# Kernel tuning notes

Measured on AMD Instinct MI355X. Metric: run time of the kernel, lower is better.

The kernel has to match this reference:

```python
import jax, jax.numpy as jnp
import numpy as np

B, N, D = 8, 2048, 256
TOP_K_INST = 512
TOP_K_REL = 32
EPS = 1e-5  # F.layer_norm default eps


def setup_inputs() -> dict:
    key = jax.random.key(0)
    kq, kk = jax.random.split(key)
    q = jax.random.normal(kq, (B, N, D), dtype=jnp.float32)
    k = jax.random.normal(kk, (B, N, D), dtype=jnp.float32)
    return {"q": q, "k": k}


def _forward(q, k):
    # raw attention scores [B,N,N] (returned un-normalized, like scores1 in torch)
    scores1 = jnp.einsum('bid,bjd->bij', q, k)
    probs = jax.nn.softmax(scores1, axis=-1)
    # top-k instances by softmax self-score on the diagonal, sorted ascending
    diag = jnp.diagonal(probs, axis1=-2, axis2=-1)                      # [B,N]
    inst_idx = jnp.sort(jax.lax.top_k(diag, TOP_K_INST)[1], axis=-1)    # [B,K]
    # gather selected rows then selected columns -> [B,K,K]
    sel = jnp.take_along_axis(probs, inst_idx[:, :, None], axis=1)      # [B,K,N]
    rel = jnp.take_along_axis(sel, inst_idx[:, None, :], axis=2)        # [B,K,K]
    # mask diagonal with large value (torch uses 1e9) before relationship topk
    rel = jnp.where(jnp.eye(TOP_K_INST, dtype=bool)[None, :, :], 1e9, rel)
    # top-R relationship columns per row; torch.where recovers them in
    # ascending column order, so sort to match
    rel_idx = jnp.sort(jax.lax.top_k(rel, TOP_K_REL)[1], axis=-1)       # [B,K,R]
    b, K, R = rel_idx.shape
    rows = jnp.broadcast_to(jnp.arange(K)[None, :, None], (b, K, R)).reshape(b, K * R)
    cols = rel_idx.reshape(b, K * R)
    subj = jnp.take_along_axis(inst_idx, rows, axis=-1)                 # [B,K*R]
    obj = jnp.take_along_axis(inst_idx, cols, axis=-1)                  # [B,K*R]
    batch_ids = jnp.broadcast_to(jnp.arange(b)[:, None], (b, K * R))
    soi = jnp.stack([batch_ids, subj, obj], axis=-1)                    # [B,K*R,3]
    # relationship embeds: q[subject] + q[object], then layernorm (no affine)
    subj_e = jnp.take_along_axis(q, subj[:, :, None], axis=1)           # [B,K*R,D]
    obj_e = jnp.take_along_axis(q, obj[:, :, None], axis=1)
    rel_e = subj_e + obj_e
    mu = jnp.mean(rel_e, axis=-1, keepdims=True)
    var = jnp.var(rel_e, axis=-1, keepdims=True)  # biased, matches F.layer_norm
    rel_e = (rel_e - mu) * jax.lax.rsqrt(var + EPS)
    return scores1, soi, rel_e


def reference(q, k):
    return _forward(q, k)
```

## Files before the change

### kernel.cpp

```cpp
#include <hip/hip_runtime.h>
#include <math.h>

#define BATCH 8
#define N 2048
#define D 256
#define K_INST 512
#define K_REL 32
#define PAIRS_PER_B (K_INST * K_REL)

__device__ __forceinline__ unsigned short f2h_u(float f) {
  _Float16 h = (_Float16)f;
  return __builtin_bit_cast(unsigned short, h);
}
__device__ __forceinline__ float h2f_u(unsigned short u) {
  return (float)__builtin_bit_cast(_Float16, u);
}

__global__ __launch_bounds__(256)
void split_f16(const float* __restrict__ q, const float* __restrict__ k,
               unsigned short* __restrict__ qh, unsigned short* __restrict__ ql,
               unsigned short* __restrict__ kh, unsigned short* __restrict__ kl) {
  const int E4 = BATCH * N * D / 4;
  for (int i = blockIdx.x * blockDim.x + threadIdx.x; i < 2 * E4;
       i += gridDim.x * blockDim.x) {
    const bool isK = i >= E4;
    const int j = isK ? (i - E4) : i;
    const float4 v = ((const float4*)(isK ? k : q))[j];
    ushort4 h, l;
    h.x = f2h_u(v.x); h.y = f2h_u(v.y); h.z = f2h_u(v.z); h.w = f2h_u(v.w);
    l.x = f2h_u(2048.0f * (v.x - h2f_u(h.x)));
    l.y = f2h_u(2048.0f * (v.y - h2f_u(h.y)));
    l.z = f2h_u(2048.0f * (v.z - h2f_u(h.z)));
    l.w = f2h_u(2048.0f * (v.w - h2f_u(h.w)));
    ((ushort4*)(isK ? kh : qh))[j] = h;
    ((ushort4*)(isK ? kl : ql))[j] = l;
  }
}

#define TM 128
#define TN 128
#define TK 32

typedef _Float16 f16x8 __attribute__((ext_vector_type(8)));
typedef float f32x4 __attribute__((ext_vector_type(4)));

__device__ __forceinline__ void load_lds16(const void* g, void* l) {
  __builtin_amdgcn_global_load_lds(
      (const __attribute__((address_space(1))) void*)g,
      (__attribute__((address_space(3))) void*)l, 16, 0, 0);
}

__global__ __launch_bounds__(256, 3)
void gemm_qkT_mfma(const unsigned short* __restrict__ qh,
                   const unsigned short* __restrict__ ql,
                   const unsigned short* __restrict__ kh,
                   const unsigned short* __restrict__ kl,
                   float* __restrict__ out) {
  const int bz = blockIdx.z;
  const int row0 = blockIdx.y * TM;
  const int col0 = blockIdx.x * TN;
  const size_t tb = (size_t)bz * N * D;

  __shared__ unsigned short Ah[TM * TK], Al[TM * TK], Bh[TM * TK], Bl[TM * TK];

  const int tid = threadIdx.x;
  const int lane = tid & 63;
  const int w = tid >> 6;
  const int wr = w >> 1, wc = w & 1;
  const int fr = lane & 15;
  const int g = lane >> 4;
  const int slot8 = ((g ^ (lane & 3)) << 3);

  int r_st[2], k_st[2];
#pragma unroll
  for (int i = 0; i < 2; i++) {
    const int b = ((w * 2 + i) << 10) + lane * 16;
    const int r = b >> 6;
    const int s = (b >> 4) & 3;
    r_st[i] = r;
    k_st[i] = (s ^ (r & 3)) * 8;
  }

  f32x4 acc[4][4];
#pragma unroll
  for (int m = 0; m < 4; m++)
#pragma unroll
    for (int n = 0; n < 4; n++) acc[m][n] = (f32x4){0.f, 0.f, 0.f, 0.f};
  const f32x4 zero4 = (f32x4){0.f, 0.f, 0.f, 0.f};
  const float inv2048 = 1.0f / 2048.0f;

  for (int kt = 0; kt < D; kt += TK) {
    __syncthreads();
#pragma unroll
    for (int i = 0; i < 2; i++) {
      const size_t aoff = tb + (size_t)(row0 + r_st[i]) * D + kt + k_st[i];
      const size_t boff = tb + (size_t)(col0 + r_st[i]) * D + kt + k_st[i];
      unsigned short* const la = &Ah[(w * 2 + i) * 512];
      unsigned short* const lA = &Al[(w * 2 + i) * 512];
      unsigned short* const lb = &Bh[(w * 2 + i) * 512];
      unsigned short* const lB = &Bl[(w * 2 + i) * 512];
      load_lds16(qh + aoff, la);
      load_lds16(ql + aoff, lA);
      load_lds16(kh + boff, lb);
      load_lds16(kl + boff, lB);
    }
    __syncthreads();

    f16x8 ah[4], al[4];
#pragma unroll
    for (int m = 0; m < 4; m++) {
      const int idx = (wr * 64 + m * 16 + fr) * TK + slot8;
      ah[m] = *(const f16x8*)&Ah[idx];
      al[m] = *(const f16x8*)&Al[idx];
    }
#pragma unroll
    for (int n = 0; n < 4; n++) {
      const int idx = (wc * 64 + n * 16 + fr) * TK + slot8;
      const f16x8 bhf = *(const f16x8*)&Bh[idx];
      const f16x8 blf = *(const f16x8*)&Bl[idx];
#pragma unroll
      for (int m = 0; m < 4; m++) {
        f32x4 t = __builtin_amdgcn_mfma_f32_16x16x32_f16(ah[m], blf, zero4, 0, 0, 0);
        t = __builtin_amdgcn_mfma_f32_16x16x32_f16(al[m], bhf, t, 0, 0, 0);
        acc[m][n] = __builtin_amdgcn_mfma_f32_16x16x32_f16(ah[m], bhf, acc[m][n], 0, 0, 0);
        acc[m][n] += t * inv2048;
      }
    }
  }

  float* O = out + (size_t)bz * N * N;
#pragma unroll
  for (int m = 0; m < 4; m++) {
#pragma unroll
    for (int r4 = 0; r4 < 4; r4++) {
      float* orow =
          &O[(size_t)(row0 + wr * 64 + m * 16 + g * 4 + r4) * N + col0 + wc * 64 + fr];
#pragma unroll
      for (int n = 0; n < 4; n++) orow[n * 16] = acc[m][n][r4];
    }
  }
}

__global__ __launch_bounds__(256)
void row_stats(const float* __restrict__ scores, float* __restrict__ m_out,
               float* __restrict__ s_out, float* __restrict__ diag_out) {
  const int row = blockIdx.x;
  const float* srow = scores + (size_t)row * N;
  const float4* r4 = (const float4*)srow;
  const int t = threadIdx.x;
  const int lane = t & 63, wid = t >> 6;
  float4 v0 = r4[t];
  float4 v1 = r4[t + 256];
  float mx = fmaxf(fmaxf(fmaxf(v0.x, v0.y), fmaxf(v0.z, v0.w)),
                   fmaxf(fmaxf(v1.x, v1.y), fmaxf(v1.z, v1.w)));
  __shared__ float redm[4], reds[4], bc[1];
#pragma unroll
  for (int o = 32; o > 0; o >>= 1) mx = fmaxf(mx, __shfl_down(mx, o));
  if (lane == 0) redm[wid] = mx;
  __syncthreads();
  if (t == 0) bc[0] = fmaxf(fmaxf(redm[0], redm[1]), fmaxf(redm[2], redm[3]));
  __syncthreads();
  const float m = bc[0];
  float s = expf(v0.x - m) + expf(v0.y - m) + expf(v0.z - m) + expf(v0.w - m)
          + expf(v1.x - m) + expf(v1.y - m) + expf(v1.z - m) + expf(v1.w - m);
#pragma unroll
  for (int o = 32; o > 0; o >>= 1) s += __shfl_down(s, o);
  if (lane == 0) reds[wid] = s;
  __syncthreads();
  if (t == 0) {
    float S = reds[0] + reds[1] + reds[2] + reds[3];
    int i = row & (N - 1);
    float sii = srow[i];
    m_out[row] = m;
    s_out[row] = S;
    diag_out[row] = expf(sii - m) / S;
  }
}

__global__ __launch_bounds__(1024)
void topk_inst(const float* __restrict__ diag, int* __restrict__ inst) {
  const int b = blockIdx.x;
  __shared__ float v[2048];
  __shared__ int id[2048];
  __shared__ int sel[K_INST];
  const int tid = threadIdx.x;
  for (int e = tid; e < 2048; e += 1024) { v[e] = diag[b * N + e]; id[e] = e; }
  __syncthreads();
  for (int k = 2; k <= 2048; k <<= 1) {
    for (int j = k >> 1; j > 0; j >>= 1) {
      const int p = tid;
      int i = 2 * p - (p & (j - 1));
      int ixj = i | j;
      float va = v[i], vb = v[ixj];
      int ia = id[i], ib = id[ixj];
      bool a_first = (va > vb) || (va == vb && ia < ib);
      bool up = ((i & k) == 0);
      if (up != a_first) { v[i] = vb; v[ixj] = va; id[i] = ib; id[ixj] = ia; }
      __syncthreads();
    }
  }
  if (tid < K_INST) sel[tid] = id[tid];
  __syncthreads();
  for (int k = 2; k <= K_INST; k <<= 1) {
    for (int j = k >> 1; j > 0; j >>= 1) {
      if (tid < 256) {
        int p = tid;
        int i = 2 * p - (p & (j - 1));
        int ixj = i | j;
        int a = sel[i], c = sel[ixj];
        bool a_first = a < c;
        bool up = ((i & k) == 0);
        if (up != a_first) { sel[i] = c; sel[ixj] = a; }
      }
      __syncthreads();
    }
  }
  if (tid < K_INST) inst[b * K_INST + tid] = sel[tid];
}

__global__ __launch_bounds__(256)
void rel_topk(const float* __restrict__ scores, const float* __restrict__ m_arr,
              const float* __restrict__ s_arr, const int* __restrict__ inst,
              float* __restrict__ soi_out, int* __restrict__ pairs) {
  const int blk = blockIdx.x;
  const int b = blk >> 9;
  const int r = blk & 511;
  __shared__ float v[K_INST];
  __shared__ int c[K_INST];
  __shared__ int selc[K_REL];
  __shared__ int sortedc[K_REL];
  const int tid = threadIdx.x;
  const int subj = inst[b * K_INST + r];
  const int rowg = b * N + subj;
  const float m = m_arr[rowg];
  const float S = s_arr[rowg];
  const float* srow = scores + (size_t)rowg * N;
  for (int e = tid; e < K_INST; e += 256) {
    int col = inst[b * K_INST + e];
    v[e] = (e == r) ? 1e9f : expf(srow[col] - m) / S;
    c[e] = e;
  }
  __syncthreads();
  for (int k = 2; k <= K_INST; k <<= 1) {
    for (int j = k >> 1; j > 0; j >>= 1) {
      int p = tid;
      int i = 2 * p - (p & (j - 1));
      int ixj = i | j;
      float va = v[i], vb = v[ixj];
      int ia = c[i], ib = c[ixj];
      bool a_first = (va > vb) || (va == vb && ia < ib);
      bool up = ((i & k) == 0);
      if (up != a_first) { v[i] = vb; v[ixj] = va; c[i] = ib; c[ixj] = ia; }
      __syncthreads();
    }
  }
  if (tid < K_REL) selc[tid] = c[tid];
  __syncthreads();
  if (tid < K_REL) {
    int myc = selc[tid];
    int rank = 0;
#pragma unroll
    for (int p2 = 0; p2 < K_REL; p2++) rank += (selc[p2] < myc);
    sortedc[rank] = myc;
  }
  __syncthreads();
  if (tid < K_REL) {
    int cc = sortedc[tid];
    int obj = inst[b * K_INST + cc];
    size_t pidx = (size_t)b * PAIRS_PER_B + (size_t)r * K_REL + tid;
    soi_out[pidx * 3 + 0] = (float)b;
    soi_out[pidx * 3 + 1] = (float)subj;
    soi_out[pidx * 3 + 2] = (float)obj;
    pairs[pidx * 2 + 0] = subj;
    pairs[pidx * 2 + 1] = obj;
  }
}

__global__ __launch_bounds__(256)
void rel_embed(const float* __restrict__ q, const int* __restrict__ pairs,
               float* __restrict__ out) {
  const size_t p = (size_t)blockIdx.x * 4 + (threadIdx.x >> 6);
  const int lane = threadIdx.x & 63;
  const int b = (int)(p >> 14);
  const int subj = pairs[p * 2], obj = pairs[p * 2 + 1];
  const float* qs = q + ((size_t)b * N + subj) * D;
  const float* qo = q + ((size_t)b * N + obj) * D;
  const float4 a = *(const float4*)(qs + lane * 4);
  const float4 c = *(const float4*)(qo + lane * 4);
  float4 e = make_float4(a.x + c.x, a.y + c.y, a.z + c.z, a.w + c.w);
  float s = e.x + e.y + e.z + e.w;
#pragma unroll
  for (int o = 32; o > 0; o >>= 1) s += __shfl_down(s, o);
  const float mu = __shfl(s, 0) * (1.0f / D);
  float4 dv = make_float4(e.x - mu, e.y - mu, e.z - mu, e.w - mu);
  float s2 = dv.x * dv.x + dv.y * dv.y + dv.z * dv.z + dv.w * dv.w;
#pragma unroll
  for (int o = 32; o > 0; o >>= 1) s2 += __shfl_down(s2, o);
  const float var = __shfl(s2, 0) * (1.0f / D);
  const float r = rsqrtf(var + 1e-5f);
  *(float4*)(out + p * D + lane * 4) =
      make_float4(dv.x * r, dv.y * r, dv.z * r, dv.w * r);
}

extern "C" void kernel_launch(void* const* d_in, const int* in_sizes, int n_in,
                              void* d_out, int out_size, void* d_ws, size_t ws_size,
                              hipStream_t stream) {
  const float* q = (const float*)d_in[0];
  const float* k = (const float*)d_in[1];
  float* out = (float*)d_out;

  float* scores = out;
  float* soi = out + (size_t)BATCH * N * N;
  float* rele = soi + (size_t)BATCH * PAIRS_PER_B * 3;

  float* m_arr = (float*)d_ws;
  float* s_arr = m_arr + BATCH * N;
  float* diag = s_arr + BATCH * N;
  int* inst = (int*)(diag + BATCH * N);
  int* pairs = inst + BATCH * K_INST;

  unsigned short* qh = (unsigned short*)rele;
  unsigned short* ql = qh + (size_t)BATCH * N * D;
  unsigned short* kh = ql + (size_t)BATCH * N * D;
  unsigned short* kl = kh + (size_t)BATCH * N * D;

  split_f16<<<4096, 256, 0, stream>>>(q, k, qh, ql, kh, kl);
  gemm_qkT_mfma<<<dim3(N / TN, N / TM, BATCH), 256, 0, stream>>>(qh, ql, kh, kl, scores);
  row_stats<<<BATCH * N, 256, 0, stream>>>(scores, m_arr, s_arr, diag);
  topk_inst<<<BATCH, 1024, 0, stream>>>(diag, inst);
  rel_topk<<<BATCH * K_INST, 256, 0, stream>>>(scores, m_arr, s_arr, inst, soi, pairs);
  rel_embed<<<BATCH * PAIRS_PER_B / 4, 256, 0, stream>>>(q, pairs, rele);
}
```

Measured before the change: 423.5 us.

## Fold split-f16 scaling into a pre-scaled Q copy and sort raw-score keys

The split-precision GEMM now stores an extra Q high-part copy pre-scaled by 2048. All three MFMAs can then accumulate into a single accumulator, with one rescale at the store, instead of a temporary chain plus a vector multiply-add per tile. This costs extra global traffic and LDS for the fifth operand. The relationship top-k now sorts packed 64-bit order-preserving keys built from raw scores, since softmax is monotonic per row, which drops the exp/divide and the separate index arrays.

```diff
diff --git a/kernel.cpp b/kernel.cpp
--- a/kernel.cpp
+++ b/kernel.cpp
@@ -18,8 +18,9 @@
 
 __global__ __launch_bounds__(256)
 void split_f16(const float* __restrict__ q, const float* __restrict__ k,
-               unsigned short* __restrict__ qh, unsigned short* __restrict__ ql,
-               unsigned short* __restrict__ kh, unsigned short* __restrict__ kl) {
+               unsigned short* __restrict__ qhs, unsigned short* __restrict__ qh,
+               unsigned short* __restrict__ ql, unsigned short* __restrict__ kh,
+               unsigned short* __restrict__ kl) {
   const int E4 = BATCH * N * D / 4;
   for (int i = blockIdx.x * blockDim.x + threadIdx.x; i < 2 * E4;
        i += gridDim.x * blockDim.x) {
@@ -32,8 +33,19 @@
     l.y = f2h_u(2048.0f * (v.y - h2f_u(h.y)));
     l.z = f2h_u(2048.0f * (v.z - h2f_u(h.z)));
     l.w = f2h_u(2048.0f * (v.w - h2f_u(h.w)));
-    ((ushort4*)(isK ? kh : qh))[j] = h;
-    ((ushort4*)(isK ? kl : ql))[j] = l;
+    if (isK) {
+      ((ushort4*)kh)[j] = h;
+      ((ushort4*)kl)[j] = l;
+    } else {
+      ushort4 hs;
+      hs.x = f2h_u(2048.0f * h2f_u(h.x));
+      hs.y = f2h_u(2048.0f * h2f_u(h.y));
+      hs.z = f2h_u(2048.0f * h2f_u(h.z));
+      hs.w = f2h_u(2048.0f * h2f_u(h.w));
+      ((ushort4*)qhs)[j] = hs;
+      ((ushort4*)qh)[j] = h;
+      ((ushort4*)ql)[j] = l;
+    }
   }
 }
 
@@ -51,7 +63,8 @@
 }
 
 __global__ __launch_bounds__(256, 3)
-void gemm_qkT_mfma(const unsigned short* __restrict__ qh,
+void gemm_qkT_mfma(const unsigned short* __restrict__ qhs,
+                   const unsigned short* __restrict__ qh,
                    const unsigned short* __restrict__ ql,
                    const unsigned short* __restrict__ kh,
                    const unsigned short* __restrict__ kl,
@@ -61,7 +74,8 @@
   const int col0 = blockIdx.x * TN;
   const size_t tb = (size_t)bz * N * D;
 
-  __shared__ unsigned short Ah[TM * TK], Al[TM * TK], Bh[TM * TK], Bl[TM * TK];
+  __shared__ unsigned short Ahs[TM * TK], Ah[TM * TK], Al[TM * TK],
+                            Bh[TM * TK], Bl[TM * TK];
 
   const int tid = threadIdx.x;
   const int lane = tid & 63;
@@ -86,8 +100,6 @@
   for (int m = 0; m < 4; m++)
 #pragma unroll
     for (int n = 0; n < 4; n++) acc[m][n] = (f32x4){0.f, 0.f, 0.f, 0.f};
-  const f32x4 zero4 = (f32x4){0.f, 0.f, 0.f, 0.f};
-  const float inv2048 = 1.0f / 2048.0f;
 
   for (int kt = 0; kt < D; kt += TK) {
     __syncthreads();
@@ -95,21 +107,20 @@
     for (int i = 0; i < 2; i++) {
       const size_t aoff = tb + (size_t)(row0 + r_st[i]) * D + kt + k_st[i];
       const size_t boff = tb + (size_t)(col0 + r_st[i]) * D + kt + k_st[i];
-      unsigned short* const la = &Ah[(w * 2 + i) * 512];
-      unsigned short* const lA = &Al[(w * 2 + i) * 512];
-      unsigned short* const lb = &Bh[(w * 2 + i) * 512];
-      unsigned short* const lB = &Bl[(w * 2 + i) * 512];
-      load_lds16(qh + aoff, la);
-      load_lds16(ql + aoff, lA);
-      load_lds16(kh + boff, lb);
-      load_lds16(kl + boff, lB);
+      const int ldsoff = (w * 2 + i) * 512;
+      load_lds16(qhs + aoff, &Ahs[ldsoff]);
+      load_lds16(qh  + aoff, &Ah[ldsoff]);
+      load_lds16(ql  + aoff, &Al[ldsoff]);
+      load_lds16(kh  + boff, &Bh[ldsoff]);
+      load_lds16(kl  + boff, &Bl[ldsoff]);
     }
     __syncthreads();
 
-    f16x8 ah[4], al[4];
+    f16x8 ahs[4], ah[4], al[4];
 #pragma unroll
     for (int m = 0; m < 4; m++) {
       const int idx = (wr * 64 + m * 16 + fr) * TK + slot8;
+      ahs[m] = *(const f16x8*)&Ahs[idx];
       ah[m] = *(const f16x8*)&Ah[idx];
       al[m] = *(const f16x8*)&Al[idx];
     }
@@ -120,15 +131,15 @@
       const f16x8 blf = *(const f16x8*)&Bl[idx];
 #pragma unroll
       for (int m = 0; m < 4; m++) {
-        f32x4 t = __builtin_amdgcn_mfma_f32_16x16x32_f16(ah[m], blf, zero4, 0, 0, 0);
-        t = __builtin_amdgcn_mfma_f32_16x16x32_f16(al[m], bhf, t, 0, 0, 0);
-        acc[m][n] = __builtin_amdgcn_mfma_f32_16x16x32_f16(ah[m], bhf, acc[m][n], 0, 0, 0);
-        acc[m][n] += t * inv2048;
+        acc[m][n] = __builtin_amdgcn_mfma_f32_16x16x32_f16(ahs[m], bhf, acc[m][n], 0, 0, 0);
+        acc[m][n] = __builtin_amdgcn_mfma_f32_16x16x32_f16(ah[m], blf, acc[m][n], 0, 0, 0);
+        acc[m][n] = __builtin_amdgcn_mfma_f32_16x16x32_f16(al[m], bhf, acc[m][n], 0, 0, 0);
       }
     }
   }
 
   float* O = out + (size_t)bz * N * N;
+  const float inv2048 = 1.0f / 2048.0f;
 #pragma unroll
   for (int m = 0; m < 4; m++) {
 #pragma unroll
@@ -136,7 +147,7 @@
       float* orow =
           &O[(size_t)(row0 + wr * 64 + m * 16 + g * 4 + r4) * N + col0 + wc * 64 + fr];
 #pragma unroll
-      for (int n = 0; n < 4; n++) orow[n * 16] = acc[m][n][r4];
+      for (int n = 0; n < 4; n++) orow[n * 16] = acc[m][n][r4] * inv2048;
     }
   }
 }
@@ -219,26 +230,27 @@
 }
 
 __global__ __launch_bounds__(256)
-void rel_topk(const float* __restrict__ scores, const float* __restrict__ m_arr,
-              const float* __restrict__ s_arr, const int* __restrict__ inst,
+void rel_topk(const float* __restrict__ scores, const int* __restrict__ inst,
               float* __restrict__ soi_out, int* __restrict__ pairs) {
   const int blk = blockIdx.x;
   const int b = blk >> 9;
   const int r = blk & 511;
-  __shared__ float v[K_INST];
-  __shared__ int c[K_INST];
+  __shared__ unsigned long long kv[K_INST];
   __shared__ int selc[K_REL];
   __shared__ int sortedc[K_REL];
   const int tid = threadIdx.x;
   const int subj = inst[b * K_INST + r];
-  const int rowg = b * N + subj;
-  const float m = m_arr[rowg];
-  const float S = s_arr[rowg];
-  const float* srow = scores + (size_t)rowg * N;
+  const float* srow = scores + ((size_t)b * N + subj) * N;
   for (int e = tid; e < K_INST; e += 256) {
-    int col = inst[b * K_INST + e];
-    v[e] = (e == r) ? 1e9f : expf(srow[col] - m) / S;
-    c[e] = e;
+    unsigned int fb;
+    if (e == r) {
+      fb = 0xFFFFFFFFu;
+    } else {
+      const int col = inst[b * K_INST + e];
+      unsigned int u = __float_as_uint(srow[col]);
+      fb = (u >> 31) ? ~u : (u | 0x80000000u);
+    }
+    kv[e] = ((unsigned long long)fb << 32) | (unsigned int)(K_INST - 1 - e);
   }
   __syncthreads();
   for (int k = 2; k <= K_INST; k <<= 1) {
@@ -246,15 +258,14 @@
       int p = tid;
       int i = 2 * p - (p & (j - 1));
       int ixj = i | j;
-      float va = v[i], vb = v[ixj];
-      int ia = c[i], ib = c[ixj];
-      bool a_first = (va > vb) || (va == vb && ia < ib);
+      unsigned long long a = kv[i], c = kv[ixj];
       bool up = ((i & k) == 0);
-      if (up != a_first) { v[i] = vb; v[ixj] = va; c[i] = ib; c[ixj] = ia; }
+      if (up == (a < c)) { kv[i] = c; kv[ixj] = a; }
       __syncthreads();
     }
   }
-  if (tid < K_REL) selc[tid] = c[tid];
+  if (tid < K_REL)
+    selc[tid] = K_INST - 1 - (int)(kv[tid] & 0xFFFFFFFFu);
   __syncthreads();
   if (tid < K_REL) {
     int myc = selc[tid];
@@ -319,15 +330,16 @@
   int* inst = (int*)(diag + BATCH * N);
   int* pairs = inst + BATCH * K_INST;
 
-  unsigned short* qh = (unsigned short*)rele;
+  unsigned short* qhs = (unsigned short*)rele;
+  unsigned short* qh = qhs + (size_t)BATCH * N * D;
   unsigned short* ql = qh + (size_t)BATCH * N * D;
   unsigned short* kh = ql + (size_t)BATCH * N * D;
   unsigned short* kl = kh + (size_t)BATCH * N * D;
 
-  split_f16<<<4096, 256, 0, stream>>>(q, k, qh, ql, kh, kl);
-  gemm_qkT_mfma<<<dim3(N / TN, N / TM, BATCH), 256, 0, stream>>>(qh, ql, kh, kl, scores);
+  split_f16<<<4096, 256, 0, stream>>>(q, k, qhs, qh, ql, kh, kl);
+  gemm_qkT_mfma<<<dim3(N / TN, N / TM, BATCH), 256, 0, stream>>>(qhs, qh, ql, kh, kl, scores);
   row_stats<<<BATCH * N, 256, 0, stream>>>(scores, m_arr, s_arr, diag);
   topk_inst<<<BATCH, 1024, 0, stream>>>(diag, inst);
-  rel_topk<<<BATCH * K_INST, 256, 0, stream>>>(scores, m_arr, s_arr, inst, soi, pairs);
+  rel_topk<<<BATCH * K_INST, 256, 0, stream>>>(scores, inst, soi, pairs);
   rel_embed<<<BATCH * PAIRS_PER_B / 4, 256, 0, stream>>>(q, pairs, rele);
 }
```

Result: no change. 420.9 us (-0.6%).
